# Performance work log

Hardware: AMD Instinct MI355X
Metric: run time of the kernel (lower is better)

Reference implementation:

```python
import jax, jax.numpy as jnp
import numpy as np

N_QUBITS = 16
N_LAYERS = 4
N_ACTIONS = 6
BATCH = 512


def _apply_1q(state, U, wire):
    """Apply a single-qubit gate U to `wire` of batched state [B,2,...,2].
    U is [2,2] (shared) or [B,2,2] (per-sample)."""
    s = jnp.moveaxis(state, wire + 1, -1)
    if U.ndim == 2:
        s = jnp.einsum('ij,b...j->b...i', U, s)
    else:
        s = jnp.einsum('bij,b...j->b...i', U, s)
    return jnp.moveaxis(s, -1, wire + 1)


def _ry(theta):
    # RY(theta); theta scalar or [B]
    c = jnp.cos(theta / 2).astype(jnp.complex64)
    s = jnp.sin(theta / 2).astype(jnp.complex64)
    return jnp.stack([jnp.stack([c, -s], -1), jnp.stack([s, c], -1)], -2)


def _rot(phi, theta, omega):
    # PennyLane Rot = RZ(omega) RY(theta) RZ(phi)
    c = jnp.cos(theta / 2)
    s = jnp.sin(theta / 2)
    ep = jnp.exp(-0.5j * (phi + omega).astype(jnp.complex64))
    em = jnp.exp(-0.5j * (phi - omega).astype(jnp.complex64))
    m00 = ep * c
    m01 = -jnp.conj(em) * s
    m10 = em * s
    m11 = jnp.conj(ep) * c
    return jnp.stack([jnp.stack([m00, m01], -1), jnp.stack([m10, m11], -1)], -2)


def _cz_factor(wire):
    # diagonal CZ phase on wires (wire, wire+1): diag(1,1,1,-1)
    f = jnp.array([1, 1, 1, -1], dtype=jnp.complex64).reshape(2, 2)
    shape = (1,) + (1,) * wire + (2, 2) + (1,) * (N_QUBITS - wire - 2)
    return f.reshape(shape)


def _circuit(x, weights):
    # x: [B, n_qubits] angles; weights: [L, n_qubits, 3]
    B = x.shape[0]
    state = jnp.zeros((B,) + (2,) * N_QUBITS, dtype=jnp.complex64)
    state = state.at[(slice(None),) + (0,) * N_QUBITS].set(1.0)
    # AngleEmbedding: RY(x_i) on wire i (per-sample angles)
    for i in range(N_QUBITS):
        state = _apply_1q(state, _ry(x[:, i]), i)
    for l in range(N_LAYERS):
        for i in range(N_QUBITS):
            state = _apply_1q(state, _rot(weights[l, i, 0], weights[l, i, 1], weights[l, i, 2]), i)
        for i in range(N_QUBITS - 1):
            state = state * _cz_factor(i)
    probs = state.real ** 2 + state.imag ** 2  # [B,2,...,2]
    zs = []
    all_axes = tuple(range(1, N_QUBITS + 1))
    for i in range(N_QUBITS):
        pi = jnp.sum(probs, axis=tuple(a for a in all_axes if a != i + 1))  # [B,2]
        zs.append(pi[:, 0] - pi[:, 1])
    return jnp.stack(zs, axis=-1)  # [B, n_qubits] expval <Z_i>


def setup_inputs() -> dict:
    key = jax.random.key(0)
    k1, k2, k3, k4 = jax.random.split(key, 4)
    x = jax.random.uniform(k1, (BATCH, N_QUBITS), dtype=jnp.float32) * np.float32(np.pi)
    weights = jax.random.normal(k2, (N_LAYERS, N_QUBITS, 3), dtype=jnp.float32)
    fc_w = jax.random.normal(k3, (N_ACTIONS, N_QUBITS), dtype=jnp.float32) / np.float32(np.sqrt(N_QUBITS))
    fc_b = jax.random.normal(k4, (N_ACTIONS,), dtype=jnp.float32) * 0.01
    return {"x": x, "weights": weights, "fc_w": fc_w, "fc_b": fc_b}


def reference(x, weights, fc_w, fc_b):
    z = _circuit(x, weights).astype(jnp.float32)  # [B, n_qubits]
    return z @ fc_w.T + fc_b  # [B, n_actions]
```

## Files before the change

### kernel.cpp

```cpp
#include <hip/hip_runtime.h>

#define NQ 16
#define NA 6
#define BATCH 512


__global__ __launch_bounds__(1024, 8)
void qdqn_kernel(const float* __restrict__ x,
                 const float* __restrict__ wt,
                 const float* __restrict__ fw,
                 const float* __restrict__ fb,
                 float* __restrict__ out)
{
    __shared__ float4 vec[22];
    __shared__ float4 g2[22][2];
    __shared__ float4 g3[22][2];
    __shared__ float4 meas[16];
    __shared__ float  zsh[NQ];

    const int tid  = threadIdx.x;
    const int b    = blockIdx.x;
    const int lane = tid & 63;
    const int wv   = tid >> 6;

    if (wv == 0) {
        if (lane < 22) {
            const int w = lane - 3;
            float4 r = make_float4(1.0f, 0.0f, 0.0f, 0.0f);
            if (0 <= w && w < NQ) {
                float sp, cp, st, ct, sx, cx;
                __sincosf(0.5f * wt[w * 3 + 0], &sp, &cp);
                __sincosf(0.5f * wt[w * 3 + 1], &st, &ct);
                __sincosf(0.5f * x[b * NQ + w], &sx, &cx);
                r = make_float4(cp * (ct * cx - st * sx), -sp * (ct * cx + st * sx),
                                cp * (st * cx + ct * sx),  sp * (ct * sx - st * cx));
            }
            vec[lane] = r;
        }
    } else if (wv == 1) {
        if (lane < 22) {
            const int w = lane - 3;
            float4 R0 = make_float4(1.0f, 0.0f, 0.0f, 0.0f);
            float4 R1 = make_float4(1.0f, 0.0f, 0.0f, 0.0f);
            if (0 <= w && w < NQ) {
                const float al = wt[(0 * NQ + w) * 3 + 2] + wt[(1 * NQ + w) * 3 + 0];
                const float th = wt[(1 * NQ + w) * 3 + 1];
                float sa, ca, st, ct;
                __sincosf(0.5f * al, &sa, &ca);
                __sincosf(0.5f * th, &st, &ct);
                R0 = make_float4(ct * ca, -ct * sa, -st * ca, -st * sa);
                R1 = make_float4(ct * ca,  ct * sa,  st * ca, -st * sa);
            }
            g2[lane][0] = R0; g2[lane][1] = R1;
        }
    } else if (wv == 2) {
        if (lane < 22) {
            const int w = lane - 3;
            float4 R0 = make_float4(1.0f, 0.0f, 0.0f, 0.0f);
            float4 R1 = make_float4(1.0f, 0.0f, 0.0f, 0.0f);
            if (0 <= w && w < NQ) {
                const float al = wt[(1 * NQ + w) * 3 + 2] + wt[(2 * NQ + w) * 3 + 0];
                const float th = wt[(2 * NQ + w) * 3 + 1];
                float sa, ca, st, ct;
                __sincosf(0.5f * al, &sa, &ca);
                __sincosf(0.5f * th, &st, &ct);
                R0 = make_float4(ct * ca, -ct * sa, -st * ca, -st * sa);
                R1 = make_float4(ct * ca,  ct * sa,  st * ca, -st * sa);
            }
            g3[lane][0] = R0; g3[lane][1] = R1;
        }
    } else if (wv == 3) {
        if (lane < NQ) {
            const int w = lane;
            const float th = wt[(3 * NQ + w) * 3 + 1];
            const float al = wt[(2 * NQ + w) * 3 + 2] + wt[(3 * NQ + w) * 3 + 0];
            float s4, c4, sa, ca;
            __sincosf(th, &s4, &c4);
            __sincosf(al, &sa, &ca);
            meas[w] = make_float4(c4, -s4 * ca, -s4 * sa, 0.0f);
        }
    }
    __syncthreads();

    const int qi = wv;

    float Pr, Pi;
    {
        const float2* vp = reinterpret_cast<const float2*>(vec);
        float2 f = vp[((qi + 1) << 1) + (lane & 1)];
        Pr = f.x; Pi = f.y;
#pragma unroll
        for (int j = 2; j <= 6; ++j) {
            const float2 g = vp[((qi + j) << 1) + ((lane >> (j - 1)) & 1)];
            const float nr = Pr * g.x - Pi * g.y;
            const float ni = Pr * g.y + Pi * g.x;
            Pr = nr; Pi = ni;
        }
    }
    const float4 v0 = vec[qi];
    float ar0 = Pr * v0.x - Pi * v0.y, ai0 = Pr * v0.y + Pi * v0.x;
    float ar1 = Pr * v0.z - Pi * v0.w, ai1 = Pr * v0.w + Pi * v0.z;

    const int n0 = lane << 1, n1 = n0 | 1;
    const float czs0 = (__popc((n0 & (n0 >> 1)) & 0x3F) & 1) ? -1.0f : 1.0f;
    const float czs1 = (__popc((n1 & (n1 >> 1)) & 0x3F) & 1) ? -1.0f : 1.0f;

#define CZ() do { ar0 *= czs0; ai0 *= czs0; ar1 *= czs1; ai1 *= czs1; } while (0)
#define GATE(J, ARR) do {                                                      \
    const int  m_   = 1 << ((J) - 1);                                          \
    const int  row_ = (lane >> ((J) - 1)) & 1;                                 \
    const float4 c  = ARR[qi + (J)][row_];                                     \
    const float pr0 = __shfl_xor(ar0, m_, 64);                                 \
    const float pi0 = __shfl_xor(ai0, m_, 64);                                 \
    const float pr1 = __shfl_xor(ar1, m_, 64);                                 \
    const float pi1 = __shfl_xor(ai1, m_, 64);                                 \
    const float t0r = c.x*ar0 - c.y*ai0 + c.z*pr0 - c.w*pi0;                   \
    const float t0i = c.x*ai0 + c.y*ar0 + c.z*pi0 + c.w*pr0;                   \
    const float t1r = c.x*ar1 - c.y*ai1 + c.z*pr1 - c.w*pi1;                   \
    const float t1i = c.x*ai1 + c.y*ar1 + c.z*pi1 + c.w*pr1;                   \
    ar0 = t0r; ai0 = t0i; ar1 = t1r; ai1 = t1i;                                \
} while (0)

    CZ();
    GATE(1, g2); GATE(2, g2); GATE(3, g2); GATE(4, g2); GATE(5, g2);
    CZ();
    GATE(2, g3); GATE(3, g3); GATE(4, g3);
    CZ();

#undef GATE
#undef CZ

    const float4 m  = meas[qi];
    const float sgn3 = ((lane >> 2) & 1) ? -1.0f : 1.0f;
    const float pr0 = __shfl_xor(ar0, 4, 64);
    const float pi0 = __shfl_xor(ai0, 4, 64);
    const float pr1 = __shfl_xor(ar1, 4, 64);
    const float pi1 = __shfl_xor(ai1, 4, 64);
    const float u  = ar0 * pr0 + ai0 * pi0 + ar1 * pr1 + ai1 * pi1;
    const float v  = ar0 * pi0 - ai0 * pr0 + ar1 * pi1 - ai1 * pr1;
    float p = sgn3 * (m.x * (ar0*ar0 + ai0*ai0 + ar1*ar1 + ai1*ai1) - m.z * v)
            + m.y * u;

#pragma unroll
    for (int off = 32; off > 0; off >>= 1)
        p += __shfl_xor(p, off, 64);
    if (lane == 0) zsh[qi] = p;
    __syncthreads();

    if (tid < NA) {
        float acc = fb[tid];
#pragma unroll
        for (int i = 0; i < NQ; ++i)
            acc += zsh[i] * fw[tid * NQ + i];
        out[b * NA + tid] = acc;
    }
}

extern "C" void kernel_launch(void* const* d_in, const int* in_sizes, int n_in,
                              void* d_out, int out_size, void* d_ws, size_t ws_size,
                              hipStream_t stream) {
    const float* x    = (const float*)d_in[0];
    const float* wts  = (const float*)d_in[1];
    const float* fc_w = (const float*)d_in[2];
    const float* fc_b = (const float*)d_in[3];
    float* out = (float*)d_out;

    qdqn_kernel<<<BATCH, 1024, 0, stream>>>(x, wts, fc_w, fc_b, out);
}
```

Before: 63.90 us.

## Process two qubit light-cones per wave and fold the last layer gates into measurement

Each wavefront now handles two target qubits (wv and wv+8), so the block shrinks from 1024 to 512 threads, and the two independent shuffle/FMA chains are interleaved for ILP. The third-layer gate on wire 3 and the final CZ are folded algebraically into precomputed measurement coefficients (measA/measB), which drops one gate application per qubit. The initial product-state amplitude is computed as a balanced tree instead of a serial chain. The aim is fewer threads and waves per block and less dependent latency, at the cost of more registers per thread and more complex setup math in wave 3.

```diff
diff --git a/kernel.cpp b/kernel.cpp
--- a/kernel.cpp
+++ b/kernel.cpp
@@ -5,7 +5,7 @@
 #define BATCH 512
 
 
-__global__ __launch_bounds__(1024, 8)
+__global__ __launch_bounds__(512, 4)
 void qdqn_kernel(const float* __restrict__ x,
                  const float* __restrict__ wt,
                  const float* __restrict__ fw,
@@ -15,7 +15,8 @@
     __shared__ float4 vec[22];
     __shared__ float4 g2[22][2];
     __shared__ float4 g3[22][2];
-    __shared__ float4 meas[16];
+    __shared__ float4 measA[16];
+    __shared__ float4 measB[16];
     __shared__ float  zsh[NQ];
 
     const int tid  = threadIdx.x;
@@ -72,79 +73,144 @@
     } else if (wv == 3) {
         if (lane < NQ) {
             const int w = lane;
-            const float th = wt[(3 * NQ + w) * 3 + 1];
-            const float al = wt[(2 * NQ + w) * 3 + 2] + wt[(3 * NQ + w) * 3 + 0];
-            float s4, c4, sa, ca;
-            __sincosf(th, &s4, &c4);
-            __sincosf(al, &sa, &ca);
-            meas[w] = make_float4(c4, -s4 * ca, -s4 * sa, 0.0f);
+            float st, ct, sb, cb, s4, c4, sa, ca;
+            __sincosf(0.5f * wt[(2 * NQ + w) * 3 + 1], &st, &ct);
+            __sincosf(0.5f * (wt[(1 * NQ + w) * 3 + 2] + wt[(2 * NQ + w) * 3 + 0]), &sb, &cb);
+            __sincosf(wt[(3 * NQ + w) * 3 + 1], &s4, &c4);
+            __sincosf(wt[(2 * NQ + w) * 3 + 2] + wt[(3 * NQ + w) * 3 + 0], &sa, &ca);
+            const float G00r =  ct * cb, G00i = -ct * sb;
+            const float G01r = -st * cb, G01i = -st * sb;
+            const float G10r =  st * cb, G10i = -st * sb;
+            const float G11r =  ct * cb, G11i =  ct * sb;
+            const float M01r = -s4 * ca, M01i = -s4 * sa;
+            const float a1  = c4 * ((G00r*G00r + G00i*G00i) - (G10r*G10r + G10i*G10i));
+            const float b1r = c4 * ((G00r*G01r + G00i*G01i) - (G10r*G11r + G10i*G11i));
+            const float b1i = c4 * ((G00r*G01i - G00i*G01r) - (G10r*G11i - G10i*G11r));
+            const float tr = G00r*G10r + G00i*G10i, ti = G00r*G10i - G00i*G10r;
+            const float a2 = 2.0f * (M01r * tr - M01i * ti);
+            const float u1r = G00r*G11r + G00i*G11i, u1i = G00r*G11i - G00i*G11r;
+            const float u2r = G10r*G01r + G10i*G01i, u2i = G10r*G01i - G10i*G01r;
+            const float b2r = (M01r*u1r - M01i*u1i) + (M01r*u2r + M01i*u2i);
+            const float b2i = (M01r*u1i + M01i*u1r) + (M01r*u2i - M01i*u2r);
+            measA[w] = make_float4(a1, b1r, b1i, a2);
+            measB[w] = make_float4(b2r, b2i, 0.0f, 0.0f);
         }
     }
     __syncthreads();
 
-    const int qi = wv;
-
-    float Pr, Pi;
-    {
-        const float2* vp = reinterpret_cast<const float2*>(vec);
-        float2 f = vp[((qi + 1) << 1) + (lane & 1)];
-        Pr = f.x; Pi = f.y;
-#pragma unroll
-        for (int j = 2; j <= 6; ++j) {
-            const float2 g = vp[((qi + j) << 1) + ((lane >> (j - 1)) & 1)];
-            const float nr = Pr * g.x - Pi * g.y;
-            const float ni = Pr * g.y + Pi * g.x;
-            Pr = nr; Pi = ni;
-        }
-    }
-    const float4 v0 = vec[qi];
-    float ar0 = Pr * v0.x - Pi * v0.y, ai0 = Pr * v0.y + Pi * v0.x;
-    float ar1 = Pr * v0.z - Pi * v0.w, ai1 = Pr * v0.w + Pi * v0.z;
+    const int qiA = wv;
+    const int qiB = wv + 8;
 
     const int n0 = lane << 1, n1 = n0 | 1;
     const float czs0 = (__popc((n0 & (n0 >> 1)) & 0x3F) & 1) ? -1.0f : 1.0f;
     const float czs1 = (__popc((n1 & (n1 >> 1)) & 0x3F) & 1) ? -1.0f : 1.0f;
 
-#define CZ() do { ar0 *= czs0; ai0 *= czs0; ar1 *= czs1; ai1 *= czs1; } while (0)
-#define GATE(J, ARR) do {                                                      \
+    const float2* vp = reinterpret_cast<const float2*>(vec);
+    float Ar0, Ai0, Ar1, Ai1, Br0, Bi0, Br1, Bi1;
+    {
+        const int i1 = (lane & 1), i2 = ((lane >> 1) & 1), i3 = ((lane >> 2) & 1);
+        const int i4 = ((lane >> 3) & 1), i5 = ((lane >> 4) & 1), i6 = ((lane >> 5) & 1);
+#define PINIT(QI, r0, s0, r1, s1) do {                                          \
+        const float2 f1 = vp[(((QI) + 1) << 1) + i1];                           \
+        const float2 f2 = vp[(((QI) + 2) << 1) + i2];                           \
+        const float2 f3 = vp[(((QI) + 3) << 1) + i3];                           \
+        const float2 f4 = vp[(((QI) + 4) << 1) + i4];                           \
+        const float2 f5 = vp[(((QI) + 5) << 1) + i5];                           \
+        const float2 f6 = vp[(((QI) + 6) << 1) + i6];                           \
+        const float t12r = f1.x*f2.x - f1.y*f2.y, t12i = f1.x*f2.y + f1.y*f2.x; \
+        const float t34r = f3.x*f4.x - f3.y*f4.y, t34i = f3.x*f4.y + f3.y*f4.x; \
+        const float t56r = f5.x*f6.x - f5.y*f6.y, t56i = f5.x*f6.y + f5.y*f6.x; \
+        const float q_r = t12r*t34r - t12i*t34i, q_i = t12r*t34i + t12i*t34r;   \
+        const float Pr = q_r*t56r - q_i*t56i,    Pi = q_r*t56i + q_i*t56r;      \
+        const float4 v0 = vec[QI];                                              \
+        r0 = Pr*v0.x - Pi*v0.y; s0 = Pr*v0.y + Pi*v0.x;                         \
+        r1 = Pr*v0.z - Pi*v0.w; s1 = Pr*v0.w + Pi*v0.z;                         \
+    } while (0)
+        PINIT(qiA, Ar0, Ai0, Ar1, Ai1);
+        PINIT(qiB, Br0, Bi0, Br1, Bi1);
+#undef PINIT
+    }
+
+#define CZ2X() do {                                                            \
+    Ar0 *= czs0; Ai0 *= czs0; Ar1 *= czs1; Ai1 *= czs1;                        \
+    Br0 *= czs0; Bi0 *= czs0; Br1 *= czs1; Bi1 *= czs1;                        \
+} while (0)
+
+#define GATE2(J, ARR) do {                                                     \
     const int  m_   = 1 << ((J) - 1);                                          \
     const int  row_ = (lane >> ((J) - 1)) & 1;                                 \
-    const float4 c  = ARR[qi + (J)][row_];                                     \
-    const float pr0 = __shfl_xor(ar0, m_, 64);                                 \
-    const float pi0 = __shfl_xor(ai0, m_, 64);                                 \
-    const float pr1 = __shfl_xor(ar1, m_, 64);                                 \
-    const float pi1 = __shfl_xor(ai1, m_, 64);                                 \
-    const float t0r = c.x*ar0 - c.y*ai0 + c.z*pr0 - c.w*pi0;                   \
-    const float t0i = c.x*ai0 + c.y*ar0 + c.z*pi0 + c.w*pr0;                   \
-    const float t1r = c.x*ar1 - c.y*ai1 + c.z*pr1 - c.w*pi1;                   \
-    const float t1i = c.x*ai1 + c.y*ar1 + c.z*pi1 + c.w*pr1;                   \
-    ar0 = t0r; ai0 = t0i; ar1 = t1r; ai1 = t1i;                                \
+    const float4 cA = ARR[qiA + (J)][row_];                                    \
+    const float4 cB = ARR[qiB + (J)][row_];                                    \
+    const float Apr0 = __shfl_xor(Ar0, m_, 64);                                \
+    const float Api0 = __shfl_xor(Ai0, m_, 64);                                \
+    const float Apr1 = __shfl_xor(Ar1, m_, 64);                                \
+    const float Api1 = __shfl_xor(Ai1, m_, 64);                                \
+    const float Bpr0 = __shfl_xor(Br0, m_, 64);                                \
+    const float Bpi0 = __shfl_xor(Bi0, m_, 64);                                \
+    const float Bpr1 = __shfl_xor(Br1, m_, 64);                                \
+    const float Bpi1 = __shfl_xor(Bi1, m_, 64);                                \
+    float t0r, t0i, t1r, t1i;                                                  \
+    t0r = cA.x*Ar0 - cA.y*Ai0 + cA.z*Apr0 - cA.w*Api0;                         \
+    t0i = cA.x*Ai0 + cA.y*Ar0 + cA.z*Api0 + cA.w*Apr0;                         \
+    t1r = cA.x*Ar1 - cA.y*Ai1 + cA.z*Apr1 - cA.w*Api1;                         \
+    t1i = cA.x*Ai1 + cA.y*Ar1 + cA.z*Api1 + cA.w*Apr1;                         \
+    Ar0 = t0r; Ai0 = t0i; Ar1 = t1r; Ai1 = t1i;                                \
+    t0r = cB.x*Br0 - cB.y*Bi0 + cB.z*Bpr0 - cB.w*Bpi0;                         \
+    t0i = cB.x*Bi0 + cB.y*Br0 + cB.z*Bpi0 + cB.w*Bpr0;                         \
+    t1r = cB.x*Br1 - cB.y*Bi1 + cB.z*Bpr1 - cB.w*Bpi1;                         \
+    t1i = cB.x*Bi1 + cB.y*Br1 + cB.z*Bpi1 + cB.w*Bpr1;                         \
+    Br0 = t0r; Bi0 = t0i; Br1 = t1r; Bi1 = t1i;                                \
 } while (0)
 
-    CZ();
-    GATE(1, g2); GATE(2, g2); GATE(3, g2); GATE(4, g2); GATE(5, g2);
-    CZ();
-    GATE(2, g3); GATE(3, g3); GATE(4, g3);
-    CZ();
-
-#undef GATE
-#undef CZ
-
-    const float4 m  = meas[qi];
-    const float sgn3 = ((lane >> 2) & 1) ? -1.0f : 1.0f;
-    const float pr0 = __shfl_xor(ar0, 4, 64);
-    const float pi0 = __shfl_xor(ai0, 4, 64);
-    const float pr1 = __shfl_xor(ar1, 4, 64);
-    const float pi1 = __shfl_xor(ai1, 4, 64);
-    const float u  = ar0 * pr0 + ai0 * pi0 + ar1 * pr1 + ai1 * pi1;
-    const float v  = ar0 * pi0 - ai0 * pr0 + ar1 * pi1 - ai1 * pr1;
-    float p = sgn3 * (m.x * (ar0*ar0 + ai0*ai0 + ar1*ar1 + ai1*ai1) - m.z * v)
-            + m.y * u;
+    CZ2X();
+    GATE2(1, g2); GATE2(2, g2); GATE2(3, g2); GATE2(4, g2); GATE2(5, g2);
+    CZ2X();
+    GATE2(2, g3); GATE2(4, g3);
+
+#undef GATE2
+#undef CZ2X
+
+    const float sgn_lr = (((lane >> 1) ^ (lane >> 3)) & 1) ? -1.0f : 1.0f;
+    const float sgnm   = ((lane >> 2) & 1) ? -1.0f : 1.0f;
+
+    const float4 mA_A = measA[qiA], mB_A = measB[qiA];
+    const float4 mA_B = measA[qiB], mB_B = measB[qiB];
+
+    const float Apr0 = __shfl_xor(Ar0, 4, 64);
+    const float Api0 = __shfl_xor(Ai0, 4, 64);
+    const float Apr1 = __shfl_xor(Ar1, 4, 64);
+    const float Api1 = __shfl_xor(Ai1, 4, 64);
+    const float Bpr0 = __shfl_xor(Br0, 4, 64);
+    const float Bpi0 = __shfl_xor(Bi0, 4, 64);
+    const float Bpr1 = __shfl_xor(Br1, 4, 64);
+    const float Bpi1 = __shfl_xor(Bi1, 4, 64);
+
+    float pA, pB;
+    {
+        const float aE  = fmaf(sgn_lr, mA_A.w, mA_A.x);
+        const float bEr = fmaf(sgn_lr, mB_A.x, mA_A.y);
+        const float bEi = fmaf(sgn_lr, mB_A.y, mA_A.z);
+        const float nn = Ar0*Ar0 + Ai0*Ai0 + Ar1*Ar1 + Ai1*Ai1;
+        const float u  = Ar0*Apr0 + Ai0*Api0 + Ar1*Apr1 + Ai1*Api1;
+        const float v  = Ar0*Api0 - Ai0*Apr0 + Ar1*Api1 - Ai1*Apr1;
+        pA = sgnm * (aE * nn - bEi * v) + bEr * u;
+    }
+    {
+        const float aE  = fmaf(sgn_lr, mA_B.w, mA_B.x);
+        const float bEr = fmaf(sgn_lr, mB_B.x, mA_B.y);
+        const float bEi = fmaf(sgn_lr, mB_B.y, mA_B.z);
+        const float nn = Br0*Br0 + Bi0*Bi0 + Br1*Br1 + Bi1*Bi1;
+        const float u  = Br0*Bpr0 + Bi0*Bpi0 + Br1*Bpr1 + Bi1*Bpi1;
+        const float v  = Br0*Bpi0 - Bi0*Bpr0 + Br1*Bpi1 - Bi1*Bpr1;
+        pB = sgnm * (aE * nn - bEi * v) + bEr * u;
+    }
 
 #pragma unroll
-    for (int off = 32; off > 0; off >>= 1)
-        p += __shfl_xor(p, off, 64);
-    if (lane == 0) zsh[qi] = p;
+    for (int off = 32; off > 0; off >>= 1) {
+        pA += __shfl_xor(pA, off, 64);
+        pB += __shfl_xor(pB, off, 64);
+    }
+    if (lane == 0) { zsh[qiA] = pA; zsh[qiB] = pB; }
     __syncthreads();
 
     if (tid < NA) {
@@ -165,5 +231,5 @@
     const float* fc_b = (const float*)d_in[3];
     float* out = (float*)d_out;
 
-    qdqn_kernel<<<BATCH, 1024, 0, stream>>>(x, wts, fc_w, fc_b, out);
+    qdqn_kernel<<<BATCH, 512, 0, stream>>>(x, wts, fc_w, fc_b, out);
 }
```

Measured after the change: 63.05 us. Within noise of the previous version (-1.3%).

## Pack two samples per block with 8 amplitudes per lane and fold last layer into measurement

Applied to the files above, without the earlier changes.

Each block now handles two batch samples with 512 threads. Every qubit's light-cone state is spread over 16 lanes holding 8 complex amplitudes each, instead of 64 lanes holding 2, so several gates run in-register with no cross-lane shuffles. The last layer's Rot gate and the final CZ are folded analytically into precomputed measurement coefficients, which removes work from the per-lane chain. The cost is more registers per thread and extra setup math done by a single wave.

```diff
diff --git a/kernel.cpp b/kernel.cpp
--- a/kernel.cpp
+++ b/kernel.cpp
@@ -5,27 +5,29 @@
 #define BATCH 512
 
 
-__global__ __launch_bounds__(1024, 8)
+__global__ __launch_bounds__(512)
 void qdqn_kernel(const float* __restrict__ x,
                  const float* __restrict__ wt,
                  const float* __restrict__ fw,
                  const float* __restrict__ fb,
                  float* __restrict__ out)
 {
-    __shared__ float4 vec[22];
+    __shared__ float4 vec2[2][22];
     __shared__ float4 g2[22][2];
     __shared__ float4 g3[22][2];
-    __shared__ float4 meas[16];
-    __shared__ float  zsh[NQ];
+    __shared__ float4 measA[16];
+    __shared__ float4 measB[16];
+    __shared__ float  zsh[2][NQ];
 
     const int tid  = threadIdx.x;
-    const int b    = blockIdx.x;
+    const int blk  = blockIdx.x;
     const int lane = tid & 63;
     const int wv   = tid >> 6;
 
-    if (wv == 0) {
+    if ((wv & 3) == 0) {
         if (lane < 22) {
             const int w = lane - 3;
+            const int b = 2 * blk + (wv >> 2);
             float4 r = make_float4(1.0f, 0.0f, 0.0f, 0.0f);
             if (0 <= w && w < NQ) {
                 float sp, cp, st, ct, sx, cx;
@@ -35,7 +37,7 @@
                 r = make_float4(cp * (ct * cx - st * sx), -sp * (ct * cx + st * sx),
                                 cp * (st * cx + ct * sx),  sp * (ct * sx - st * cx));
             }
-            vec[lane] = r;
+            vec2[wv >> 2][lane] = r;
         }
     } else if (wv == 1) {
         if (lane < 22) {
@@ -72,87 +74,164 @@
     } else if (wv == 3) {
         if (lane < NQ) {
             const int w = lane;
-            const float th = wt[(3 * NQ + w) * 3 + 1];
-            const float al = wt[(2 * NQ + w) * 3 + 2] + wt[(3 * NQ + w) * 3 + 0];
-            float s4, c4, sa, ca;
-            __sincosf(th, &s4, &c4);
-            __sincosf(al, &sa, &ca);
-            meas[w] = make_float4(c4, -s4 * ca, -s4 * sa, 0.0f);
+            float st, ct, sb, cb, s4, c4, sa, ca;
+            __sincosf(0.5f * wt[(2 * NQ + w) * 3 + 1], &st, &ct);
+            __sincosf(0.5f * (wt[(1 * NQ + w) * 3 + 2] + wt[(2 * NQ + w) * 3 + 0]), &sb, &cb);
+            __sincosf(wt[(3 * NQ + w) * 3 + 1], &s4, &c4);
+            __sincosf(wt[(2 * NQ + w) * 3 + 2] + wt[(3 * NQ + w) * 3 + 0], &sa, &ca);
+            const float G00r =  ct * cb, G00i = -ct * sb;
+            const float G01r = -st * cb, G01i = -st * sb;
+            const float G10r =  st * cb, G10i = -st * sb;
+            const float G11r =  ct * cb, G11i =  ct * sb;
+            const float M01r = -s4 * ca, M01i = -s4 * sa;
+            const float a1  = c4 * ((G00r*G00r + G00i*G00i) - (G10r*G10r + G10i*G10i));
+            const float b1r = c4 * ((G00r*G01r + G00i*G01i) - (G10r*G11r + G10i*G11i));
+            const float b1i = c4 * ((G00r*G01i - G00i*G01r) - (G10r*G11i - G10i*G11r));
+            const float tr = G00r*G10r + G00i*G10i, ti = G00r*G10i - G00i*G10r;
+            const float a2 = 2.0f * (M01r * tr - M01i * ti);
+            const float u1r = G00r*G11r + G00i*G11i, u1i = G00r*G11i - G00i*G11r;
+            const float u2r = G10r*G01r + G10i*G01i, u2i = G10r*G01i - G10i*G01r;
+            const float b2r = (M01r*u1r - M01i*u1i) + (M01r*u2r + M01i*u2i);
+            const float b2i = (M01r*u1i + M01i*u1r) + (M01r*u2i - M01i*u2r);
+            measA[w] = make_float4(a1, b1r, b1i, a2);
+            measB[w] = make_float4(b2r, b2i, 0.0f, 0.0f);
         }
     }
     __syncthreads();
 
-    const int qi = wv;
-
-    float Pr, Pi;
+    const int sid = wv >> 2;
+    const int qi  = ((wv & 3) << 2) | ((lane >> 4) & 3);
+    const int ln  = lane & 15;
+    const float4* vecS = vec2[sid];
+
+    float sr[8], si[8];
+
     {
-        const float2* vp = reinterpret_cast<const float2*>(vec);
-        float2 f = vp[((qi + 1) << 1) + (lane & 1)];
-        Pr = f.x; Pi = f.y;
+        const float2* vp = reinterpret_cast<const float2*>(vecS);
+        const float2 f3 = vp[((qi + 3) << 1) + (ln & 1)];
+        const float2 f4 = vp[((qi + 4) << 1) + ((ln >> 1) & 1)];
+        const float2 f5 = vp[((qi + 5) << 1) + ((ln >> 2) & 1)];
+        const float2 f6 = vp[((qi + 6) << 1) + ((ln >> 3) & 1)];
+        const float t34r = f3.x*f4.x - f3.y*f4.y, t34i = f3.x*f4.y + f3.y*f4.x;
+        const float t56r = f5.x*f6.x - f5.y*f6.y, t56i = f5.x*f6.y + f5.y*f6.x;
+        const float Pcr  = t34r*t56r - t34i*t56i, Pci  = t34r*t56i + t34i*t56r;
+        const float4 v0 = vecS[qi], v1 = vecS[qi + 1], v2 = vecS[qi + 2];
+        const float e00r = v0.x*v1.x - v0.y*v1.y, e00i = v0.x*v1.y + v0.y*v1.x;
+        const float e10r = v0.z*v1.x - v0.w*v1.y, e10i = v0.z*v1.y + v0.w*v1.x;
+        const float e01r = v0.x*v1.z - v0.y*v1.w, e01i = v0.x*v1.w + v0.y*v1.z;
+        const float e11r = v0.z*v1.z - v0.w*v1.w, e11i = v0.z*v1.w + v0.w*v1.z;
+        const float g0r = Pcr*v2.x - Pci*v2.y, g0i = Pcr*v2.y + Pci*v2.x;
+        const float g1r = Pcr*v2.z - Pci*v2.w, g1i = Pcr*v2.w + Pci*v2.z;
+        sr[0] = e00r*g0r - e00i*g0i;  si[0] = e00r*g0i + e00i*g0r;
+        sr[1] = e10r*g0r - e10i*g0i;  si[1] = e10r*g0i + e10i*g0r;
+        sr[2] = e01r*g0r - e01i*g0i;  si[2] = e01r*g0i + e01i*g0r;
+        sr[3] = e11r*g0r - e11i*g0i;  si[3] = e11r*g0i + e11i*g0r;
+        sr[4] = e00r*g1r - e00i*g1i;  si[4] = e00r*g1i + e00i*g1r;
+        sr[5] = e10r*g1r - e10i*g1i;  si[5] = e10r*g1i + e10i*g1r;
+        sr[6] = e01r*g1r - e01i*g1i;  si[6] = e01r*g1i + e01i*g1r;
+        sr[7] = e11r*g1r - e11i*g1i;  si[7] = e11r*g1i + e11i*g1r;
+    }
+
+    const float czl = (__popc((ln & (ln >> 1)) & 7) & 1) ? -1.0f : 1.0f;
+    const float czx = (ln & 1) ? -1.0f : 1.0f;
+    const float czA = czl;
+    const float czB = czl * czx;
+
+#define CZ() do {                                                              \
+    sr[0] *=  czA; si[0] *=  czA;  sr[1] *=  czA; si[1] *=  czA;               \
+    sr[2] *=  czA; si[2] *=  czA;  sr[3] *= -czA; si[3] *= -czA;               \
+    sr[4] *=  czB; si[4] *=  czB;  sr[5] *=  czB; si[5] *=  czB;               \
+    sr[6] *= -czB; si[6] *= -czB;  sr[7] *=  czB; si[7] *=  czB;               \
+} while (0)
+
+#define INLANE_GATE(ARR, SLOT, P) do {                                         \
+    const float4 R0 = ARR[qi + (SLOT)][0];                                     \
+    const float4 R1 = ARR[qi + (SLOT)][1];                                     \
+    _Pragma("unroll")                                                          \
+    for (int r = 0; r < 8; ++r) {                                              \
+        if (((r >> (P)) & 1) == 0) {                                           \
+            const int q = r | (1 << (P));                                      \
+            const float nr0 = R0.x*sr[r] - R0.y*si[r] + R0.z*sr[q] - R0.w*si[q]; \
+            const float ni0 = R0.x*si[r] + R0.y*sr[r] + R0.z*si[q] + R0.w*sr[q]; \
+            const float nr1 = R1.z*sr[r] - R1.w*si[r] + R1.x*sr[q] - R1.y*si[q]; \
+            const float ni1 = R1.z*si[r] + R1.w*sr[r] + R1.x*si[q] + R1.y*sr[q]; \
+            sr[r] = nr0; si[r] = ni0; sr[q] = nr1; si[q] = ni1;                \
+        }                                                                      \
+    }                                                                          \
+} while (0)
+
+#define SHFL_GATE(ARR, SLOT, T) do {                                           \
+    const float4 c = ARR[qi + (SLOT)][(ln >> (T)) & 1];                        \
+    float pr[8], pi[8];                                                        \
+    _Pragma("unroll")                                                          \
+    for (int r = 0; r < 8; ++r) {                                              \
+        pr[r] = __shfl_xor(sr[r], 1 << (T), 64);                               \
+        pi[r] = __shfl_xor(si[r], 1 << (T), 64);                               \
+    }                                                                          \
+    _Pragma("unroll")                                                          \
+    for (int r = 0; r < 8; ++r) {                                              \
+        const float nr = c.x*sr[r] - c.y*si[r] + c.z*pr[r] - c.w*pi[r];        \
+        const float ni = c.x*si[r] + c.y*sr[r] + c.z*pi[r] + c.w*pr[r];        \
+        sr[r] = nr; si[r] = ni;                                                \
+    }                                                                          \
+} while (0)
+
+    CZ();
+    INLANE_GATE(g2, 1, 1);
+    INLANE_GATE(g2, 2, 2);
+    SHFL_GATE(g2, 3, 0);
+    SHFL_GATE(g2, 4, 1);
+    SHFL_GATE(g2, 5, 2);
+    CZ();
+    INLANE_GATE(g3, 2, 2);
+    SHFL_GATE(g3, 4, 1);
+
+#undef CZ
+#undef INLANE_GATE
+#undef SHFL_GATE
+
+    const float4 mA = measA[qi], mB = measB[qi];
+    const float s0 = ((ln >> 1) & 1) ? -1.0f : 1.0f;
+    const float aE_lo  = mA.x + s0 * mA.w,  aE_hi  = mA.x - s0 * mA.w;
+    const float bEr_lo = mA.y + s0 * mB.x,  bEr_hi = mA.y - s0 * mB.x;
+    const float bEi_lo = mA.z + s0 * mB.y,  bEi_hi = mA.z - s0 * mB.y;
+    const float sgnm = (ln & 1) ? -1.0f : 1.0f;
+
+    float p = 0.0f;
+    {
+        float pr[8], pi[8];
 #pragma unroll
-        for (int j = 2; j <= 6; ++j) {
-            const float2 g = vp[((qi + j) << 1) + ((lane >> (j - 1)) & 1)];
-            const float nr = Pr * g.x - Pi * g.y;
-            const float ni = Pr * g.y + Pi * g.x;
-            Pr = nr; Pi = ni;
-        }
-    }
-    const float4 v0 = vec[qi];
-    float ar0 = Pr * v0.x - Pi * v0.y, ai0 = Pr * v0.y + Pi * v0.x;
-    float ar1 = Pr * v0.z - Pi * v0.w, ai1 = Pr * v0.w + Pi * v0.z;
-
-    const int n0 = lane << 1, n1 = n0 | 1;
-    const float czs0 = (__popc((n0 & (n0 >> 1)) & 0x3F) & 1) ? -1.0f : 1.0f;
-    const float czs1 = (__popc((n1 & (n1 >> 1)) & 0x3F) & 1) ? -1.0f : 1.0f;
-
-#define CZ() do { ar0 *= czs0; ai0 *= czs0; ar1 *= czs1; ai1 *= czs1; } while (0)
-#define GATE(J, ARR) do {                                                      \
-    const int  m_   = 1 << ((J) - 1);                                          \
-    const int  row_ = (lane >> ((J) - 1)) & 1;                                 \
-    const float4 c  = ARR[qi + (J)][row_];                                     \
-    const float pr0 = __shfl_xor(ar0, m_, 64);                                 \
-    const float pi0 = __shfl_xor(ai0, m_, 64);                                 \
-    const float pr1 = __shfl_xor(ar1, m_, 64);                                 \
-    const float pi1 = __shfl_xor(ai1, m_, 64);                                 \
-    const float t0r = c.x*ar0 - c.y*ai0 + c.z*pr0 - c.w*pi0;                   \
-    const float t0i = c.x*ai0 + c.y*ar0 + c.z*pi0 + c.w*pr0;                   \
-    const float t1r = c.x*ar1 - c.y*ai1 + c.z*pr1 - c.w*pi1;                   \
-    const float t1i = c.x*ai1 + c.y*ar1 + c.z*pi1 + c.w*pr1;                   \
-    ar0 = t0r; ai0 = t0i; ar1 = t1r; ai1 = t1i;                                \
-} while (0)
-
-    CZ();
-    GATE(1, g2); GATE(2, g2); GATE(3, g2); GATE(4, g2); GATE(5, g2);
-    CZ();
-    GATE(2, g3); GATE(3, g3); GATE(4, g3);
-    CZ();
-
-#undef GATE
-#undef CZ
-
-    const float4 m  = meas[qi];
-    const float sgn3 = ((lane >> 2) & 1) ? -1.0f : 1.0f;
-    const float pr0 = __shfl_xor(ar0, 4, 64);
-    const float pi0 = __shfl_xor(ai0, 4, 64);
-    const float pr1 = __shfl_xor(ar1, 4, 64);
-    const float pi1 = __shfl_xor(ai1, 4, 64);
-    const float u  = ar0 * pr0 + ai0 * pi0 + ar1 * pr1 + ai1 * pi1;
-    const float v  = ar0 * pi0 - ai0 * pr0 + ar1 * pi1 - ai1 * pr1;
-    float p = sgn3 * (m.x * (ar0*ar0 + ai0*ai0 + ar1*ar1 + ai1*ai1) - m.z * v)
-            + m.y * u;
-
+        for (int r = 0; r < 8; ++r) {
+            pr[r] = __shfl_xor(sr[r], 1, 64);
+            pi[r] = __shfl_xor(si[r], 1, 64);
+        }
 #pragma unroll
-    for (int off = 32; off > 0; off >>= 1)
-        p += __shfl_xor(p, off, 64);
-    if (lane == 0) zsh[qi] = p;
+        for (int r = 0; r < 8; ++r) {
+            const float aE  = (r < 4) ? aE_lo  : aE_hi;
+            const float bEr = (r < 4) ? bEr_lo : bEr_hi;
+            const float bEi = (r < 4) ? bEi_lo : bEi_hi;
+            const float nn = sr[r]*sr[r] + si[r]*si[r];
+            const float u  = sr[r]*pr[r] + si[r]*pi[r];
+            const float v  = sr[r]*pi[r] - si[r]*pr[r];
+            p += sgnm * (aE * nn - bEi * v) + bEr * u;
+        }
+    }
+
+    p += __shfl_xor(p, 1, 64);
+    p += __shfl_xor(p, 2, 64);
+    p += __shfl_xor(p, 4, 64);
+    p += __shfl_xor(p, 8, 64);
+    if ((lane & 15) == 0) zsh[sid][qi] = p;
     __syncthreads();
 
-    if (tid < NA) {
-        float acc = fb[tid];
+    const int sid2 = tid >> 8;
+    const int t6   = tid & 255;
+    if (t6 < NA) {
+        float acc = fb[t6];
 #pragma unroll
         for (int i = 0; i < NQ; ++i)
-            acc += zsh[i] * fw[tid * NQ + i];
-        out[b * NA + tid] = acc;
+            acc += zsh[sid2][i] * fw[t6 * NQ + i];
+        out[(2 * blk + sid2) * NA + t6] = acc;
     }
 }
 
@@ -165,5 +244,5 @@
     const float* fc_b = (const float*)d_in[3];
     float* out = (float*)d_out;
 
-    qdqn_kernel<<<BATCH, 1024, 0, stream>>>(x, wts, fc_w, fc_b, out);
+    qdqn_kernel<<<BATCH / 2, 512, 0, stream>>>(x, wts, fc_w, fc_b, out);
 }
```

Measured after the change: 61.80 us. 1.03x faster.
